# Kernel tuning notes

Hardware: AMD Instinct MI355X
Metric: run time of the kernel (lower is better)

Reference implementation:

```python
import jax, jax.numpy as jnp
import numpy as np

N_FEATURES = 128
LENGTH = 10.0  # length_scale
N_NODES = 10000
N_EDGES = 200000


def mlp(x, W1, b1, W2, b2):
    # embedding.MLP(in, hidden, out): Linear -> SiLU -> Linear
    return jax.nn.silu(x @ W1 + b1) @ W2 + b2


def positional_encoding(dist, n_features, length):
    # sinusoidal encoding of scalar distances -> [E, n_features]
    ranks = jnp.arange(n_features // 2, dtype=dist.dtype)
    arg = dist[:, None] * ranks[None, :] * (np.pi / length)  # [E, F/2]
    return jnp.concatenate([jnp.sin(arg), jnp.cos(arg)], axis=-1)


def setup_inputs() -> dict:
    key = jax.random.key(0)
    N, E, F = N_NODES, N_EDGES, N_FEATURES
    ks = jax.random.split(key, 10)
    d = {}
    d["edge_index"] = jax.random.randint(ks[0], (2, E), 0, N)
    d["invariant_node_features"] = jax.random.normal(ks[1], (N, F), dtype=jnp.float32)
    d["equivariant_node_features"] = jax.random.normal(ks[2], (N, F, 3), dtype=jnp.float32)
    d["invariant_edge_features"] = jax.random.normal(ks[3], (E, F), dtype=jnp.float32)
    d["edge_dist"] = jax.random.uniform(ks[4], (E,), dtype=jnp.float32, minval=0.1, maxval=10.0)
    d["edge_dir"] = jax.random.normal(ks[5], (E, 3), dtype=jnp.float32)
    # phi: MLP(2F -> F -> 5F); w: MLP(F -> F -> 5F)
    d["phi_W1"] = jax.random.normal(ks[6], (2 * F, F), dtype=jnp.float32) / np.sqrt(2 * F)
    d["phi_b1"] = jnp.zeros((F,), jnp.float32)
    d["phi_W2"] = jax.random.normal(ks[7], (F, 5 * F), dtype=jnp.float32) / np.sqrt(F)
    d["phi_b2"] = jnp.zeros((5 * F,), jnp.float32)
    d["w_W1"] = jax.random.normal(ks[8], (F, F), dtype=jnp.float32) / np.sqrt(F)
    d["w_b1"] = jnp.zeros((F,), jnp.float32)
    d["w_W2"] = jax.random.normal(ks[9], (F, 5 * F), dtype=jnp.float32) / np.sqrt(F)
    d["w_b2"] = jnp.zeros((5 * F,), jnp.float32)
    return d


def reference(edge_index, invariant_node_features, equivariant_node_features,
              invariant_edge_features, edge_dist, edge_dir,
              phi_W1, phi_b1, phi_W2, phi_b2, w_W1, w_b1, w_W2, w_b2):
    F = N_FEATURES
    src, dst = edge_index[0], edge_index[1]
    # gather + concat edge features -> phi input [E, 2F]
    in_feat = jnp.concatenate([invariant_node_features[src], invariant_edge_features], axis=-1)
    pe = positional_encoding(edge_dist, F, LENGTH)  # [E, F]
    m = mlp(in_feat, phi_W1, phi_b1, phi_W2, phi_b2) * mlp(pe, w_W1, w_b1, w_W2, w_b2)  # [E, 5F]
    gates, cp_gates, scale_edge_dir, ds, de = jnp.split(m, 5, axis=-1)
    src_eq = equivariant_node_features[src]            # [E, F, 3]
    dst_eq = equivariant_node_features[dst]            # [E, F, 3]
    edir = edge_dir[:, None, :]                        # [E, 1, 3]
    # multiply_first_dim(w, x) == w[..., None] * x for [E,F] x [E,F,3]
    gated_features = gates[..., None] * src_eq
    scaled_edge_dir = scale_edge_dir[..., None] * edir
    cross = jnp.cross(jnp.broadcast_to(edir, dst_eq.shape), dst_eq)  # [E, F, 3]
    gated_cross = cp_gates[..., None] * cross
    dv = scaled_edge_dir + gated_features + gated_cross  # [E, F, 3]
    N = invariant_node_features.shape[0]
    dv = jax.ops.segment_sum(dv, dst, num_segments=N)   # [N, F, 3]
    ds = jax.ops.segment_sum(ds, dst, num_segments=N)   # [N, F]
    return (equivariant_node_features + dv,
            invariant_node_features + ds,
            invariant_edge_features + de)
```

## Files before the change

kernel.cpp:

```cpp
#include <hip/hip_runtime.h>
#include <math.h>

#define E_EDGES 200000
#define N_NODES 10000
#define FDIM    128

typedef __attribute__((ext_vector_type(8))) short  short8;
typedef __attribute__((ext_vector_type(4))) float  float4v;

#define WT1_OFF   0
#define WTW1_OFF  32768
#define WT2_OFF   49152
#define WTW2_OFF  131072
#define W_TOTAL   212992
#define CNT_BYTE  425984
#define CUR_BYTE  465984
#define PERM_BYTE 505984

#define EQ_OUT_SZ   (N_NODES * FDIM * 3)
#define INV_OUT_SZ  (N_NODES * FDIM)

__device__ __forceinline__ unsigned short f2bf(float x) {
    union { float f; unsigned u; } v; v.f = x;
    unsigned r = v.u + 0x7fffu + ((v.u >> 16) & 1u);
    return (unsigned short)(r >> 16);
}
__device__ __forceinline__ float bf2f(unsigned short h) {
    union { unsigned u; float f; } v; v.u = ((unsigned)h) << 16; return v.f;
}

__device__ __forceinline__ unsigned short* tile_ptr(unsigned short* base, int row, int col) {
    unsigned off = (unsigned)(row * 256 + col * 2);
    off ^= (unsigned)((row & 7) << 4);
    return (unsigned short*)((char*)base + off);
}
__device__ __forceinline__ float* dvs_ptr(float* base, int row, int fl, int c) {
    unsigned off = (unsigned)(row * 1024 + fl * 16 + c * 4);
    off ^= (unsigned)((row & 7) << 4);
    return (float*)((char*)base + off);
}

__global__ void prep_fused(const float* __restrict__ phiW1,
                           const float* __restrict__ wW1,
                           const float* __restrict__ phiW2,
                           const float* __restrict__ wW2,
                           unsigned short* __restrict__ ws,
                           int* __restrict__ counts,
                           const float* __restrict__ eq,
                           const float* __restrict__ inv,
                           float* __restrict__ out) {
    int t = blockIdx.x * 256 + threadIdx.x;
    if (t < N_NODES) counts[t] = 0;
    if (t < W_TOTAL) {
        if (t < 32768) {
            int n = t >> 8, k = t & 255;
            ws[WT1_OFF + t] = f2bf(phiW1[k * 128 + n]);
        } else if (t < 49152) {
            int i = t - 32768; int n = i >> 7, k = i & 127;
            ws[WTW1_OFF + i] = f2bf(wW1[k * 128 + n]);
        } else if (t < 131072) {
            int i = t - 49152; int n = i >> 7, k = i & 127;
            ws[WT2_OFF + i] = f2bf(phiW2[k * 640 + n]);
        } else {
            int i = t - 131072; int n = i >> 7, k = i & 127;
            ws[WTW2_OFF + i] = f2bf(wW2[k * 640 + n]);
        }
    }
    if (t < EQ_OUT_SZ / 4) {
        ((float4v*)out)[t] = ((const float4v*)eq)[t];
    } else {
        int u = t - EQ_OUT_SZ / 4;
        ((float4v*)(out + EQ_OUT_SZ))[u] = ((const float4v*)inv)[u];
    }
}

__global__ void hist_kernel(const int* __restrict__ eidx, int* __restrict__ counts) {
    int e = blockIdx.x * 256 + threadIdx.x;
    if (e < E_EDGES) atomicAdd(&counts[eidx[E_EDGES + e]], 1);
}
__global__ __launch_bounds__(1024)
void scan_kernel(const int* __restrict__ counts, int* __restrict__ cursor) {
    __shared__ int sums[1024];
    const int t = threadIdx.x;
    const int base = t * 10;
    int local[10];
    int s = 0;
    #pragma unroll
    for (int j = 0; j < 10; ++j) {
        int b = base + j;
        int v = (b < N_NODES) ? counts[b] : 0;
        local[j] = s; s += v;
    }
    sums[t] = s;
    __syncthreads();
    for (int off = 1; off < 1024; off <<= 1) {
        int v = (t >= off) ? sums[t - off] : 0;
        __syncthreads();
        sums[t] += v;
        __syncthreads();
    }
    int pre = (t > 0) ? sums[t - 1] : 0;
    #pragma unroll
    for (int j = 0; j < 10; ++j) {
        int b = base + j;
        if (b < N_NODES) cursor[b] = pre + local[j];
    }
}
__global__ void scatter_kernel(const int* __restrict__ eidx,
                               int* __restrict__ cursor, int* __restrict__ perm) {
    int e = blockIdx.x * 256 + threadIdx.x;
    if (e < E_EDGES) {
        int d = eidx[E_EDGES + e];
        int pos = atomicAdd(&cursor[d], 1);
        perm[pos] = e;
    }
}

__global__ __launch_bounds__(256, 3)
void edge_kernel(const int*   __restrict__ eidx,
                 const float* __restrict__ node_inv,
                 const float* __restrict__ eqf,
                 const float* __restrict__ edge_inv,
                 const float* __restrict__ dist,
                 const float* __restrict__ dir,
                 const float* __restrict__ phi_b1,
                 const float* __restrict__ phi_b2,
                 const float* __restrict__ w_b1,
                 const float* __restrict__ w_b2,
                 const unsigned short* __restrict__ wsW,
                 const int* __restrict__ perm,
                 float* __restrict__ out) {
    __shared__ __align__(16) unsigned char smem_u[32768];
    __shared__ int   s_e[32], s_src[32], s_dst[32];
    __shared__ float s_dir[32][3];
    __shared__ float s_dist[32];

    unsigned short* A1a = (unsigned short*)smem_u;
    unsigned short* A1b = (unsigned short*)(smem_u + 8192);
    unsigned short* H1  = (unsigned short*)(smem_u + 16384);
    unsigned short* H2  = (unsigned short*)(smem_u + 24576);
    float*          DVSf = (float*)smem_u;

    const int tid = threadIdx.x;
    const int p0  = blockIdx.x * 32;

    if (tid < 32) {
        int e = perm[p0 + tid];
        s_e[tid]   = e;
        s_src[tid] = eidx[e];
        s_dst[tid] = eidx[E_EDGES + e];
        s_dir[tid][0] = dir[e * 3 + 0];
        s_dir[tid][1] = dir[e * 3 + 1];
        s_dir[tid][2] = dir[e * 3 + 2];
        s_dist[tid]  = dist[e];
    }
    __syncthreads();

    {
        const int i   = tid >> 3;
        const int seg = tid & 7;
        const int k0  = seg * 32;
        const float* base;
        unsigned short* tb;
        int c0;
        if (k0 < 128) { base = node_inv + (size_t)s_src[i] * 128 + k0; tb = A1a; c0 = k0; }
        else          { base = edge_inv + (size_t)s_e[i]  * 128 + (k0 - 128); tb = A1b; c0 = k0 - 128; }
        #pragma unroll
        for (int j = 0; j < 4; ++j) {
            float4v v0 = *(const float4v*)(base + j * 8);
            float4v v1 = *(const float4v*)(base + j * 8 + 4);
            short8 sv;
            #pragma unroll
            for (int u = 0; u < 4; ++u) {
                sv[u]     = (short)f2bf(v0[u]);
                sv[u + 4] = (short)f2bf(v1[u]);
            }
            *(short8*)tile_ptr(tb, i, c0 + j * 8) = sv;
        }
    }
    __syncthreads();

    const int wv   = tid >> 6;
    const int ln   = tid & 63;
    const int l16  = ln & 15;
    const int quad = ln >> 4;

    const unsigned short* Wt1  = wsW + WT1_OFF;
    const unsigned short* Wtw1 = wsW + WTW1_OFF;
    const unsigned short* Wt2  = wsW + WT2_OFF;
    const unsigned short* Wtw2 = wsW + WTW2_OFF;

    const float4v zero4 = {0.f, 0.f, 0.f, 0.f};

    float4v acc1[2][2], acc2[2][2];
    #pragma unroll
    for (int rt = 0; rt < 2; ++rt)
        #pragma unroll
        for (int ct = 0; ct < 2; ++ct) { acc1[rt][ct] = zero4; acc2[rt][ct] = zero4; }

    #pragma unroll
    for (int kk = 0; kk < 4; ++kk) {
        const int k = kk * 32 + quad * 8;
        short8 a0 = *(const short8*)tile_ptr(A1a, l16, k);
        short8 a1 = *(const short8*)tile_ptr(A1a, 16 + l16, k);
        #pragma unroll
        for (int ct = 0; ct < 2; ++ct) {
            const int n = wv * 32 + ct * 16 + l16;
            short8 b = *(const short8*)&Wt1[n * 256 + k];
            acc1[0][ct] = __builtin_amdgcn_mfma_f32_16x16x32_bf16(a0, b, acc1[0][ct], 0, 0, 0);
            acc1[1][ct] = __builtin_amdgcn_mfma_f32_16x16x32_bf16(a1, b, acc1[1][ct], 0, 0, 0);
        }
    }
    #pragma unroll
    for (int kk = 0; kk < 4; ++kk) {
        const int k = kk * 32 + quad * 8;
        short8 a0 = *(const short8*)tile_ptr(A1b, l16, k);
        short8 a1 = *(const short8*)tile_ptr(A1b, 16 + l16, k);
        #pragma unroll
        for (int ct = 0; ct < 2; ++ct) {
            const int n = wv * 32 + ct * 16 + l16;
            short8 b = *(const short8*)&Wt1[n * 256 + 128 + k];
            acc1[0][ct] = __builtin_amdgcn_mfma_f32_16x16x32_bf16(a0, b, acc1[0][ct], 0, 0, 0);
            acc1[1][ct] = __builtin_amdgcn_mfma_f32_16x16x32_bf16(a1, b, acc1[1][ct], 0, 0, 0);
        }
    }
    {
        const float cst = 3.14159265358979323846f / 10.0f;
        const float d0 = s_dist[l16] * cst;
        const float d1 = s_dist[16 + l16] * cst;
        short8 pe0[4], pe1[4];
        #pragma unroll
        for (int kk = 0; kk < 4; ++kk) {
            short8 s0, s1;
            #pragma unroll
            for (int u = 0; u < 8; ++u) {
                const int f = kk * 32 + quad * 8 + u;
                const float fa = (float)((kk < 2) ? f : (f - 64));
                float v0, v1;
                if (kk < 2) { v0 = __sinf(d0 * fa); v1 = __sinf(d1 * fa); }
                else        { v0 = __cosf(d0 * fa); v1 = __cosf(d1 * fa); }
                s0[u] = (short)f2bf(v0);
                s1[u] = (short)f2bf(v1);
            }
            pe0[kk] = s0; pe1[kk] = s1;
        }
        #pragma unroll
        for (int kk = 0; kk < 4; ++kk) {
            const int k = kk * 32 + quad * 8;
            #pragma unroll
            for (int ct = 0; ct < 2; ++ct) {
                const int n = wv * 32 + ct * 16 + l16;
                short8 b = *(const short8*)&Wtw1[n * 128 + k];
                acc2[0][ct] = __builtin_amdgcn_mfma_f32_16x16x32_bf16(pe0[kk], b, acc2[0][ct], 0, 0, 0);
                acc2[1][ct] = __builtin_amdgcn_mfma_f32_16x16x32_bf16(pe1[kk], b, acc2[1][ct], 0, 0, 0);
            }
        }
    }
    #pragma unroll
    for (int ct = 0; ct < 2; ++ct) {
        const int n = wv * 32 + ct * 16 + l16;
        const float b1v  = phi_b1[n];
        const float bw1v = w_b1[n];
        #pragma unroll
        for (int rt = 0; rt < 2; ++rt)
            #pragma unroll
            for (int r = 0; r < 4; ++r) {
                const int row = rt * 16 + quad * 4 + r;
                float x = acc1[rt][ct][r] + b1v;
                *tile_ptr(H1, row, n) = f2bf(x / (1.f + __expf(-x)));
                float y = acc2[rt][ct][r] + bw1v;
                *tile_ptr(H2, row, n) = f2bf(y / (1.f + __expf(-y)));
            }
    }
    __syncthreads();

    float* eq_out   = out;
    float* inv_out  = out + EQ_OUT_SZ;
    float* edge_out = out + EQ_OUT_SZ + INV_OUT_SZ;

    short8 ha[2][4], hb[2][4];
    #pragma unroll
    for (int rt = 0; rt < 2; ++rt)
        #pragma unroll
        for (int kk = 0; kk < 4; ++kk) {
            const int k = kk * 32 + quad * 8;
            ha[rt][kk] = *(const short8*)tile_ptr(H1, rt * 16 + l16, k);
            hb[rt][kk] = *(const short8*)tile_ptr(H2, rt * 16 + l16, k);
        }
    unsigned short a1bv[2][8];
    #pragma unroll
    for (int fc2 = 0; fc2 < 2; ++fc2)
        #pragma unroll
        for (int rt = 0; rt < 2; ++rt)
            #pragma unroll
            for (int rr = 0; rr < 4; ++rr)
                a1bv[fc2][rt * 4 + rr] =
                    *tile_ptr(A1b, rt * 16 + quad * 4 + rr, fc2 * 64 + wv * 16 + l16);
    __syncthreads();

    const int red_f = tid >> 2;
    const int red_c = tid & 3;

    #pragma unroll
    for (int fc2 = 0; fc2 < 2; ++fc2) {
        float4v mv[2][5];
        #pragma unroll
        for (int g = 0; g < 5; ++g) {
            const int n = g * 128 + fc2 * 64 + wv * 16 + l16;
            float4v p1a = zero4, p1b = zero4, p2a = zero4, p2b = zero4;
            #pragma unroll
            for (int kk = 0; kk < 4; ++kk) {
                const int k = kk * 32 + quad * 8;
                short8 b1f = *(const short8*)&Wt2[n * 128 + k];
                short8 b2f = *(const short8*)&Wtw2[n * 128 + k];
                p1a = __builtin_amdgcn_mfma_f32_16x16x32_bf16(ha[0][kk], b1f, p1a, 0, 0, 0);
                p1b = __builtin_amdgcn_mfma_f32_16x16x32_bf16(ha[1][kk], b1f, p1b, 0, 0, 0);
                p2a = __builtin_amdgcn_mfma_f32_16x16x32_bf16(hb[0][kk], b2f, p2a, 0, 0, 0);
                p2b = __builtin_amdgcn_mfma_f32_16x16x32_bf16(hb[1][kk], b2f, p2b, 0, 0, 0);
            }
            const float b2v  = phi_b2[n];
            const float bw2v = w_b2[n];
            mv[0][g] = (p1a + b2v) * (p2a + bw2v);
            mv[1][g] = (p1b + b2v) * (p2b + bw2v);
        }
        {
            const int fl = wv * 16 + l16;
            const int fg = fc2 * 64 + fl;
            #pragma unroll
            for (int rt = 0; rt < 2; ++rt) {
                #pragma unroll
                for (int r = 0; r < 4; ++r) {
                    const int row = rt * 16 + quad * 4 + r;
                    const float gate = mv[rt][0][r];
                    const float cpg  = mv[rt][1][r];
                    const float sc   = mv[rt][2][r];
                    const float dsv  = mv[rt][3][r];
                    const float dev  = mv[rt][4][r];
                    const int sn = s_src[row], dn = s_dst[row], e = s_e[row];
                    const float ex = s_dir[row][0], ey = s_dir[row][1], ez = s_dir[row][2];
                    const float* se = eqf + ((size_t)sn * 128 + fg) * 3;
                    const float* dq = eqf + ((size_t)dn * 128 + fg) * 3;
                    const float sx = se[0], sy = se[1], sz = se[2];
                    const float dx = dq[0], dy = dq[1], dz = dq[2];
                    const float cx = ey * dz - ez * dy;
                    const float cy = ez * dx - ex * dz;
                    const float cz = ex * dy - ey * dx;
                    float4v v;
                    v[0] = sc * ex + gate * sx + cpg * cx;
                    v[1] = sc * ey + gate * sy + cpg * cy;
                    v[2] = sc * ez + gate * sz + cpg * cz;
                    v[3] = dsv;
                    *(float4v*)dvs_ptr(DVSf, row, fl, 0) = v;
                    edge_out[(size_t)e * 128 + fg] = bf2f(a1bv[fc2][rt * 4 + r]) + dev;
                }
            }
        }
        __syncthreads();
        {
            const int fgr = fc2 * 64 + red_f;
            float acc = 0.f;
            int prev = s_dst[0];
            #pragma unroll
            for (int r = 0; r < 32; ++r) {
                const int d = s_dst[r];
                const float v = *dvs_ptr(DVSf, r, red_f, red_c);
                if (d != prev) {
                    if (red_c < 3) atomicAdd(eq_out + ((size_t)prev * 128 + fgr) * 3 + red_c, acc);
                    else           atomicAdd(inv_out + (size_t)prev * 128 + fgr, acc);
                    acc = 0.f; prev = d;
                }
                acc += v;
            }
            if (red_c < 3) atomicAdd(eq_out + ((size_t)prev * 128 + fgr) * 3 + red_c, acc);
            else           atomicAdd(inv_out + (size_t)prev * 128 + fgr, acc);
        }
        __syncthreads();
    }
}

extern "C" void kernel_launch(void* const* d_in, const int* in_sizes, int n_in,
                              void* d_out, int out_size, void* d_ws, size_t ws_size,
                              hipStream_t stream) {
    const int*   eidx     = (const int*)d_in[0];
    const float* node_inv = (const float*)d_in[1];
    const float* eqf      = (const float*)d_in[2];
    const float* edge_inv = (const float*)d_in[3];
    const float* dist     = (const float*)d_in[4];
    const float* dir      = (const float*)d_in[5];
    const float* phi_W1   = (const float*)d_in[6];
    const float* phi_b1   = (const float*)d_in[7];
    const float* phi_W2   = (const float*)d_in[8];
    const float* phi_b2   = (const float*)d_in[9];
    const float* w_W1     = (const float*)d_in[10];
    const float* w_b1     = (const float*)d_in[11];
    const float* w_W2     = (const float*)d_in[12];
    const float* w_b2     = (const float*)d_in[13];
    float* out = (float*)d_out;
    unsigned short* wsW = (unsigned short*)d_ws;
    int* counts = (int*)((char*)d_ws + CNT_BYTE);
    int* cursor = (int*)((char*)d_ws + CUR_BYTE);
    int* perm   = (int*)((char*)d_ws + PERM_BYTE);

    prep_fused<<<(EQ_OUT_SZ + INV_OUT_SZ) / 4 / 256, 256, 0, stream>>>(
        phi_W1, w_W1, phi_W2, w_W2, wsW, counts, eqf, node_inv, out);
    hist_kernel<<<(E_EDGES + 255) / 256, 256, 0, stream>>>(eidx, counts);
    scan_kernel<<<1, 1024, 0, stream>>>(counts, cursor);
    scatter_kernel<<<(E_EDGES + 255) / 256, 256, 0, stream>>>(eidx, cursor, perm);
    edge_kernel<<<E_EDGES / 32, 256, 0, stream>>>(eidx, node_inv, eqf, edge_inv, dist, dir,
                                                  phi_b1, phi_b2, w_b1, w_b2, wsW, perm, out);
}
```

Baseline: 694.8 us.

## Reduce dst segments in registers via wave shuffles instead of LDS staging

Replaces the LDS staging of per-edge dv/ds values and the serial 32-row segmented scan with an in-register reduction. A ballot over sorted destination indices builds a run mask, and each wave sums each run across quads with xor shuffles before issuing atomics. This removes LDS traffic and two block barriers per feature chunk. In exchange there is a data-dependent loop with divergent run handling, and atomics are issued per 16-row half, so runs that cross the half boundary produce more atomics.

```diff
diff --git a/kernel.cpp b/kernel.cpp
--- a/kernel.cpp
+++ b/kernel.cpp
@@ -33,11 +33,6 @@
     unsigned off = (unsigned)(row * 256 + col * 2);
     off ^= (unsigned)((row & 7) << 4);
     return (unsigned short*)((char*)base + off);
-}
-__device__ __forceinline__ float* dvs_ptr(float* base, int row, int fl, int c) {
-    unsigned off = (unsigned)(row * 1024 + fl * 16 + c * 4);
-    off ^= (unsigned)((row & 7) << 4);
-    return (float*)((char*)base + off);
 }
 
 __global__ void prep_fused(const float* __restrict__ phiW1,
@@ -139,7 +134,6 @@
     unsigned short* A1b = (unsigned short*)(smem_u + 8192);
     unsigned short* H1  = (unsigned short*)(smem_u + 16384);
     unsigned short* H2  = (unsigned short*)(smem_u + 24576);
-    float*          DVSf = (float*)smem_u;
 
     const int tid = threadIdx.x;
     const int p0  = blockIdx.x * 32;
@@ -287,19 +281,13 @@
             ha[rt][kk] = *(const short8*)tile_ptr(H1, rt * 16 + l16, k);
             hb[rt][kk] = *(const short8*)tile_ptr(H2, rt * 16 + l16, k);
         }
-    unsigned short a1bv[2][8];
-    #pragma unroll
-    for (int fc2 = 0; fc2 < 2; ++fc2)
-        #pragma unroll
-        for (int rt = 0; rt < 2; ++rt)
-            #pragma unroll
-            for (int rr = 0; rr < 4; ++rr)
-                a1bv[fc2][rt * 4 + rr] =
-                    *tile_ptr(A1b, rt * 16 + quad * 4 + rr, fc2 * 64 + wv * 16 + l16);
-    __syncthreads();
-
-    const int red_f = tid >> 2;
-    const int red_c = tid & 3;
+
+    unsigned run_mask;
+    {
+        bool st = (ln < 32) && (ln == 0 || s_dst[ln] != s_dst[ln - 1]);
+        unsigned long long b = __ballot(st);
+        run_mask = (unsigned)b;
+    }
 
     #pragma unroll
     for (int fc2 = 0; fc2 < 2; ++fc2) {
@@ -323,58 +311,64 @@
             mv[0][g] = (p1a + b2v) * (p2a + bw2v);
             mv[1][g] = (p1b + b2v) * (p2b + bw2v);
         }
-        {
-            const int fl = wv * 16 + l16;
-            const int fg = fc2 * 64 + fl;
-            #pragma unroll
-            for (int rt = 0; rt < 2; ++rt) {
+        const int fl = wv * 16 + l16;
+        const int fg = fc2 * 64 + fl;
+        #pragma unroll
+        for (int rt = 0; rt < 2; ++rt) {
+            float4v v[4];
+            #pragma unroll
+            for (int r = 0; r < 4; ++r) {
+                const int row = rt * 16 + quad * 4 + r;
+                const float gate = mv[rt][0][r];
+                const float cpg  = mv[rt][1][r];
+                const float sc   = mv[rt][2][r];
+                const float dsv  = mv[rt][3][r];
+                const float dev  = mv[rt][4][r];
+                const int sn = s_src[row], dn = s_dst[row], e = s_e[row];
+                const float ex = s_dir[row][0], ey = s_dir[row][1], ez = s_dir[row][2];
+                const float* se = eqf + ((size_t)sn * 128 + fg) * 3;
+                const float* dq = eqf + ((size_t)dn * 128 + fg) * 3;
+                const float sx = se[0], sy = se[1], sz = se[2];
+                const float dx = dq[0], dy = dq[1], dz = dq[2];
+                const float cx = ey * dz - ez * dy;
+                const float cy = ez * dx - ex * dz;
+                const float cz = ex * dy - ey * dx;
+                float4v t;
+                t[0] = sc * ex + gate * sx + cpg * cx;
+                t[1] = sc * ey + gate * sy + cpg * cy;
+                t[2] = sc * ez + gate * sz + cpg * cz;
+                t[3] = dsv;
+                v[r] = t;
+                edge_out[(size_t)e * 128 + fg] = bf2f(*tile_ptr(A1b, row, fg)) + dev;
+            }
+            const int base = rt * 16;
+            unsigned s = ((run_mask >> base) & 0xFFFFu) | 1u;
+            while (s) {
+                const int lo = __ffs(s) - 1;
+                s &= s - 1;
+                const int hi = s ? (__ffs(s) - 1) : 16;
+                const int d = s_dst[base + lo];
+                float px = 0.f, py = 0.f, pz = 0.f, pw = 0.f;
                 #pragma unroll
-                for (int r = 0; r < 4; ++r) {
-                    const int row = rt * 16 + quad * 4 + r;
-                    const float gate = mv[rt][0][r];
-                    const float cpg  = mv[rt][1][r];
-                    const float sc   = mv[rt][2][r];
-                    const float dsv  = mv[rt][3][r];
-                    const float dev  = mv[rt][4][r];
-                    const int sn = s_src[row], dn = s_dst[row], e = s_e[row];
-                    const float ex = s_dir[row][0], ey = s_dir[row][1], ez = s_dir[row][2];
-                    const float* se = eqf + ((size_t)sn * 128 + fg) * 3;
-                    const float* dq = eqf + ((size_t)dn * 128 + fg) * 3;
-                    const float sx = se[0], sy = se[1], sz = se[2];
-                    const float dx = dq[0], dy = dq[1], dz = dq[2];
-                    const float cx = ey * dz - ez * dy;
-                    const float cy = ez * dx - ex * dz;
-                    const float cz = ex * dy - ey * dx;
-                    float4v v;
-                    v[0] = sc * ex + gate * sx + cpg * cx;
-                    v[1] = sc * ey + gate * sy + cpg * cy;
-                    v[2] = sc * ez + gate * sz + cpg * cz;
-                    v[3] = dsv;
-                    *(float4v*)dvs_ptr(DVSf, row, fl, 0) = v;
-                    edge_out[(size_t)e * 128 + fg] = bf2f(a1bv[fc2][rt * 4 + r]) + dev;
+                for (int rr = 0; rr < 4; ++rr) {
+                    const int rloc = quad * 4 + rr;
+                    if (rloc >= lo && rloc < hi) {
+                        px += v[rr][0]; py += v[rr][1]; pz += v[rr][2]; pw += v[rr][3];
+                    }
                 }
-            }
-        }
-        __syncthreads();
-        {
-            const int fgr = fc2 * 64 + red_f;
-            float acc = 0.f;
-            int prev = s_dst[0];
-            #pragma unroll
-            for (int r = 0; r < 32; ++r) {
-                const int d = s_dst[r];
-                const float v = *dvs_ptr(DVSf, r, red_f, red_c);
-                if (d != prev) {
-                    if (red_c < 3) atomicAdd(eq_out + ((size_t)prev * 128 + fgr) * 3 + red_c, acc);
-                    else           atomicAdd(inv_out + (size_t)prev * 128 + fgr, acc);
-                    acc = 0.f; prev = d;
+                px += __shfl_xor(px, 16); px += __shfl_xor(px, 32);
+                py += __shfl_xor(py, 16); py += __shfl_xor(py, 32);
+                pz += __shfl_xor(pz, 16); pz += __shfl_xor(pz, 32);
+                pw += __shfl_xor(pw, 16); pw += __shfl_xor(pw, 32);
+                if (quad == 0) {
+                    float* eb = eq_out + ((size_t)d * 128 + fg) * 3;
+                    atomicAdd(eb + 0, px);
+                    atomicAdd(eb + 1, py);
+                    atomicAdd(eb + 2, pz);
+                    atomicAdd(inv_out + (size_t)d * 128 + fg, pw);
                 }
-                acc += v;
-            }
-            if (red_c < 3) atomicAdd(eq_out + ((size_t)prev * 128 + fgr) * 3 + red_c, acc);
-            else           atomicAdd(inv_out + (size_t)prev * 128 + fgr, acc);
-        }
-        __syncthreads();
+            }
+        }
     }
 }
 
```

Result: slower. 783.2 us (+12.7%).
